# Kernel tuning notes

Hardware: AMD Instinct MI355X
Metric: run time of the kernel (lower is better)

Reference implementation:

```python
import jax, jax.numpy as jnp
import numpy as np

# dims
B, NB, T, NC = 16, 55, 512, 8          # batch, filter bands, time steps, CSP comps
D, L, H, E, K, F, C = 512, 6, 8, 8, 2, 2048, 2  # embed, depth, heads, experts, top_k, d_ff, classes
DH = D // H
IN = NB * NC  # 440
EPS = 1e-5


def _ln(x, s, b):
    m = x.mean(-1, keepdims=True)
    v = ((x - m) ** 2).mean(-1, keepdims=True)
    return (x - m) / jnp.sqrt(v + EPS) * s + b


def setup_inputs() -> dict:
    key = jax.random.key(0)
    ks = iter(jax.random.split(key, 64))
    n = lambda shape, s=0.02: jax.random.normal(next(ks), shape, jnp.float32) * s
    inp = {
        "x": jax.random.normal(next(ks), (B, NB, T, NC), jnp.float32),
        # frontend
        "proj_w": n((IN, D)), "proj_b": jnp.zeros((D,), jnp.float32),
        "pos": n((1, T, D)),
        "ln_pre_s": jnp.ones((D,), jnp.float32), "ln_pre_b": jnp.zeros((D,), jnp.float32),
        # stacked transformer-block params [L, ...]
        "ln1_s": jnp.ones((L, D), jnp.float32), "ln1_b": jnp.zeros((L, D), jnp.float32),
        "wq": n((L, D, D)), "bq": jnp.zeros((L, D), jnp.float32),
        "wk": n((L, D, D)), "bk": jnp.zeros((L, D), jnp.float32),
        "wv": n((L, D, D)), "bv": jnp.zeros((L, D), jnp.float32),
        "wo": n((L, D, D)), "bo": jnp.zeros((L, D), jnp.float32),
        "ln2_s": jnp.ones((L, D), jnp.float32), "ln2_b": jnp.zeros((L, D), jnp.float32),
        "gate_w": n((L, D, E)),
        "e_w1": n((L, E, D, F)), "e_b1": jnp.zeros((L, E, F), jnp.float32),
        "e_w2": n((L, E, F, D)), "e_b2": jnp.zeros((L, E, D), jnp.float32),
        # classifier head
        "ln_f_s": jnp.ones((D,), jnp.float32), "ln_f_b": jnp.zeros((D,), jnp.float32),
        "head_w": n((D, C)), "head_b": jnp.zeros((C,), jnp.float32),
    }
    return inp


def _moe(h, gw, w1, b1, w2, b2):
    # h: [N, D]; top-K softmax-gated mixture of GELU-FFN experts + load-balance aux loss
    N = h.shape[0]
    probs = jax.nn.softmax(h @ gw, axis=-1)                  # [N, E]
    vals, idx = jax.lax.top_k(probs, K)                      # [N, K]
    w = vals / vals.sum(-1, keepdims=True)                   # renormalized top-k weights
    disp = jax.nn.one_hot(idx, E, dtype=h.dtype)             # [N, K, E]
    combine = (disp * w[..., None]).sum(1)                   # [N, E]
    y = jnp.zeros_like(h)
    for e in range(E):  # small fixed expert loop
        y = y + combine[:, e:e + 1] * (jax.nn.gelu(h @ w1[e] + b1[e]) @ w2[e] + b2[e])
    frac = disp.mean((0, 1)) * K                             # fraction of tokens routed to each expert
    aux = E * jnp.sum(frac * probs.mean(0))
    return y, aux


def reference(x, proj_w, proj_b, pos, ln_pre_s, ln_pre_b, ln1_s, ln1_b, wq, bq, wk, bk,
              wv, bv, wo, bo, ln2_s, ln2_b, gate_w, e_w1, e_b1, e_w2, e_b2,
              ln_f_s, ln_f_b, head_w, head_b):
    b, nb, t, nc = x.shape
    h = x.transpose(0, 2, 1, 3).reshape(b, t, nb * nc) @ proj_w + proj_b  # [B,T,D]
    h = _ln(h + pos[:, :t, :], ln_pre_s, ln_pre_b)
    scale = DH ** -0.5
    total_aux = jnp.float32(0.0)
    for l in range(L):
        # pre-LN multi-head self-attention
        a = _ln(h, ln1_s[l], ln1_b[l])
        q = (a @ wq[l] + bq[l]).reshape(b, t, H, DH)
        k = (a @ wk[l] + bk[l]).reshape(b, t, H, DH)
        v = (a @ wv[l] + bv[l]).reshape(b, t, H, DH)
        att = jax.nn.softmax(jnp.einsum('bqhd,bkhd->bhqk', q, k) * scale, axis=-1)
        o = jnp.einsum('bhqk,bkhd->bqhd', att, v).reshape(b, t, D) @ wo[l] + bo[l]
        h = h + o
        # pre-LN MoE FFN
        m = _ln(h, ln2_s[l], ln2_b[l]).reshape(b * t, D)
        y, aux = _moe(m, gate_w[l], e_w1[l], e_b1[l], e_w2[l], e_b2[l])
        h = h + y.reshape(b, t, D)
        total_aux = total_aux + aux
    pooled = h.mean(axis=1)                                   # [B, D]
    logits = _ln(pooled, ln_f_s, ln_f_b) @ head_w + head_b    # [B, C]
    return logits, total_aux
```

## Files before the change

kernel.cpp:

```cpp
#include <hip/hip_runtime.h>
#include <stdint.h>

typedef unsigned short u16;
typedef unsigned int   u32;
typedef short bh8 __attribute__((ext_vector_type(8)));
typedef float f4  __attribute__((ext_vector_type(4)));

#define NTOK    8192
#define PADROWS 17408
#define MAXTILES 136

__device__ __forceinline__ u16 f2bf(float f){
  u32 u = __float_as_uint(f);
  return (u16)((u + 0x7fffu + ((u>>16)&1u)) >> 16);
}
__device__ __forceinline__ float bf2f(u16 h){ return __uint_as_float(((u32)h)<<16); }
__device__ __forceinline__ u32 pk2(float a, float b){ return (u32)f2bf(a) | ((u32)f2bf(b)<<16); }
__device__ __forceinline__ float gelu_f(float x){
  float u = 0.7978845608028654f*(x + 0.044715f*x*x*x);
  float t = 1.f - 2.f/(__expf(2.f*u)+1.f);
  return 0.5f*x*(1.f+t);
}
__device__ __forceinline__ void gload_lds16(const void* g, void* l){
  __builtin_amdgcn_global_load_lds((const __attribute__((address_space(1))) u32*)g,
                                   (__attribute__((address_space(3))) u32*)l, 16, 0, 0);
}

__global__ __launch_bounds__(256) void xpose_k(const float* __restrict__ x, u16* __restrict__ xt){
  int idx = blockIdx.x*256 + threadIdx.x;
  const float* src = x + (size_t)idx*8;
  float4 a = *(const float4*)src;
  float4 b = *(const float4*)(src+4);
  int t  = idx & 511;
  int nb = (idx>>9) % 55;
  int bb = (idx>>9) / 55;
  uint4 u;
  u.x = pk2(a.x,a.y); u.y = pk2(a.z,a.w); u.z = pk2(b.x,b.y); u.w = pk2(b.z,b.w);
  *(uint4*)&xt[((size_t)(bb*512+t))*448 + nb*8] = u;
}

__device__ __forceinline__ void tile_xpose(const float* __restrict__ src, u16* __restrict__ dst,
                                           int Ksrc, int N, int Kdst, float (*tile)[65])
{
  int tid = threadIdx.x;
  int k0 = blockIdx.y*64, n0 = blockIdx.x*64;
  #pragma unroll
  for (int p=0;p<4;++p){
    int r = p*16 + (tid>>4);
    int c4 = (tid&15)*4;
    int k = k0 + r;
    float4 v = (k < Ksrc) ? *(const float4*)&src[(size_t)k*N + n0 + c4] : (float4){0.f,0.f,0.f,0.f};
    tile[r][c4]=v.x; tile[r][c4+1]=v.y; tile[r][c4+2]=v.z; tile[r][c4+3]=v.w;
  }
  __syncthreads();
  #pragma unroll
  for (int p=0;p<2;++p){
    int rn = p*32 + (tid>>3);
    int ck = (tid&7)*8;
    uint4 u;
    u.x = pk2(tile[ck+0][rn], tile[ck+1][rn]);
    u.y = pk2(tile[ck+2][rn], tile[ck+3][rn]);
    u.z = pk2(tile[ck+4][rn], tile[ck+5][rn]);
    u.w = pk2(tile[ck+6][rn], tile[ck+7][rn]);
    *(uint4*)&dst[(size_t)(n0+rn)*Kdst + k0 + ck] = u;
  }
}

__global__ __launch_bounds__(256) void wconv_k(const float* __restrict__ src, u16* __restrict__ dst,
                                               int Ksrc, int N, int Kdst){
  __shared__ float tile[64][65];
  src += (size_t)blockIdx.z*Ksrc*N;
  dst += (size_t)blockIdx.z*N*Kdst;
  tile_xpose(src, dst, Ksrc, N, Kdst, tile);
}

__global__ __launch_bounds__(256) void wconvqkvo_k(const float* __restrict__ wq, const float* __restrict__ wk,
    const float* __restrict__ wv, const float* __restrict__ wo,
    u16* __restrict__ qkvt, u16* __restrict__ wot)
{
  __shared__ float tile[64][65];
  int z = blockIdx.z;
  int l = z>>2, which = z&3;
  const float* src = ((which==0)? wq : (which==1)? wk : (which==2)? wv : wo) + (size_t)l*512*512;
  u16* dst = (which==3) ? wot + (size_t)l*512*512
                        : qkvt + (size_t)l*1536*512 + (size_t)which*512*512;
  tile_xpose(src, dst, 512, 512, 512, tile);
}

__global__ __launch_bounds__(256) void qkvb_k(const float* __restrict__ bq, const float* __restrict__ bk,
                                              const float* __restrict__ bv, float* __restrict__ qkvb){
  int idx = blockIdx.x*256 + threadIdx.x;
  int l = idx/1536, c = idx - l*1536;
  const float* s = (c<512)? bq : (c<1024)? bk : bv;
  qkvb[idx] = s[l*512 + (c&511)];
}

template<int MODE, bool GATHER>
__global__ __launch_bounds__(256) void gemm2_k(
    const u16* __restrict__ A, int lda,
    const u16* __restrict__ Bt, int ldb, int Ksteps,
    const float* __restrict__ biasBase,
    float* __restrict__ Cf, u16* __restrict__ Cb, int ldc,
    const int* __restrict__ tile_e, const int* __restrict__ toklist,
    const float* __restrict__ wlist, int expN)
{
  __shared__ __align__(16) u16 SMEM[24576];
  const int tid = threadIdx.x, lane = tid&63, w = tid>>6;
  const int wr = w>>1, wc = w&1;
  int nx = gridDim.x;
  int nwg = nx * gridDim.y;
  int lin = blockIdx.y*nx + blockIdx.x;
  int qq = nwg>>3, rr = nwg&7, xc = lin&7, oo = lin>>3;
  int wg = (xc<rr ? xc*(qq+1) : rr*(qq+1)+(xc-rr)*qq) + oo;
  int by = wg/nx, bx = wg - by*nx;
  const int n0 = bx*128, m0 = by*128;
  const u16* Bp = Bt;
  const float* bias = biasBase;
  if constexpr (MODE>=3){
    int e = tile_e[by];
    Bp   += (size_t)e*(size_t)expN*(size_t)ldb;
    bias += (size_t)e*(size_t)expN;
  }
  const u16* asrc0; const u16* asrc1; const u16* bsrc0; const u16* bsrc1;
  {
    int idx0 = tid, row0 = idx0>>2, sp0 = idx0&3, ks0 = sp0 ^ ((row0>>1)&3);
    int idx1 = 256+tid, row1 = idx1>>2, sp1 = idx1&3, ks1 = sp1 ^ ((row1>>1)&3);
    size_t ar0 = GATHER ? (size_t)toklist[m0+row0] : (size_t)(m0+row0);
    size_t ar1 = GATHER ? (size_t)toklist[m0+row1] : (size_t)(m0+row1);
    asrc0 = A + ar0*(size_t)lda + ks0*8;
    asrc1 = A + ar1*(size_t)lda + ks1*8;
    bsrc0 = Bp + (size_t)(n0+row0)*ldb + ks0*8;
    bsrc1 = Bp + (size_t)(n0+row1)*ldb + ks1*8;
  }
  f4 acc[4][4];
  #pragma unroll
  for (int i=0;i<4;++i)
    #pragma unroll
    for (int j=0;j<4;++j) acc[i][j] = (f4){0.f,0.f,0.f,0.f};

  auto STAGE = [&](int kt){
    u16* bufA = SMEM + (kt%3)*8192;
    u16* bufB = bufA + 4096;
    gload_lds16(asrc0 + (size_t)kt*32, &bufA[tid*8]);
    gload_lds16(asrc1 + (size_t)kt*32, &bufA[2048 + tid*8]);
    gload_lds16(bsrc0 + (size_t)kt*32, &bufB[tid*8]);
    gload_lds16(bsrc1 + (size_t)kt*32, &bufB[2048 + tid*8]);
  };

  STAGE(0);
  if (Ksteps > 1) STAGE(1);
  if (Ksteps > 2) STAGE(2);

  for (int kt=0; kt<Ksteps; ++kt){
    int rem = Ksteps - 1 - kt;
    if (rem >= 2)      asm volatile("s_waitcnt vmcnt(8)" ::: "memory");
    else if (rem == 1) asm volatile("s_waitcnt vmcnt(4)" ::: "memory");
    else               asm volatile("s_waitcnt vmcnt(0)" ::: "memory");
    __builtin_amdgcn_s_barrier();
    u16* bufA = SMEM + (kt%3)*8192;
    u16* bufB = bufA + 4096;
    bh8 af[4], bf[4];
    const int q = lane>>4;
    #pragma unroll
    for (int mf=0;mf<4;++mf){
      int r = wr*64 + mf*16 + (lane&15);
      af[mf] = *(const bh8*)&bufA[r*32 + (q ^ ((r>>1)&3))*8];
    }
    #pragma unroll
    for (int nf=0;nf<4;++nf){
      int r = wc*64 + nf*16 + (lane&15);
      bf[nf] = *(const bh8*)&bufB[r*32 + (q ^ ((r>>1)&3))*8];
    }
    asm volatile("s_waitcnt lgkmcnt(0)" ::: "memory");
    __builtin_amdgcn_sched_barrier(0);
    __builtin_amdgcn_s_barrier();
    __builtin_amdgcn_sched_barrier(0);
    if (kt+3 < Ksteps) STAGE(kt+3);
    #pragma unroll
    for (int mf=0;mf<4;++mf)
      #pragma unroll
      for (int nf=0;nf<4;++nf)
        acc[mf][nf] = __builtin_amdgcn_mfma_f32_16x16x32_bf16(af[mf], bf[nf], acc[mf][nf], 0, 0, 0);
  }
  if constexpr (MODE==1 || MODE==3 || MODE==4){
    __syncthreads();
    u16* Cs = SMEM;
    #pragma unroll
    for (int mf=0;mf<4;++mf){
      int row0 = wr*64 + mf*16 + (lane>>4)*4;
      float wl[4];
      if constexpr (MODE==4){
        #pragma unroll
        for (int r=0;r<4;++r) wl[r] = wlist[m0+row0+r];
      }
      #pragma unroll
      for (int nf=0;nf<4;++nf){
        f4 d = acc[mf][nf];
        int col = wc*64 + nf*16 + (lane&15);
        float bv = bias[n0+col];
        #pragma unroll
        for (int r=0;r<4;++r){
          float val = d[r] + bv;
          if constexpr (MODE==3) val = gelu_f(val);
          if constexpr (MODE==4) val = wl[r]*val;
          Cs[(row0+r)*136 + col] = f2bf(val);
        }
      }
    }
    __syncthreads();
    #pragma unroll
    for (int p=0;p<8;++p){
      int idx = p*256 + tid;
      int row = idx>>4, c4 = idx&15;
      bh8 v = *(const bh8*)&Cs[row*136 + c4*8];
      int mrow = m0 + row;
      if constexpr (MODE==1){
        int nc = n0 + c4*8;
        int slab = nc>>6, dh = nc&63;
        *(bh8*)&Cb[((size_t)slab*NTOK + (size_t)mrow)*64 + dh] = v;
      } else {
        *(bh8*)&Cb[(size_t)mrow*ldc + n0 + c4*8] = v;
      }
    }
  } else {
    #pragma unroll
    for (int mf=0;mf<4;++mf){
      #pragma unroll
      for (int nf=0;nf<4;++nf){
        f4 d = acc[mf][nf];
        int ncol = n0 + wc*64 + nf*16 + (lane&15);
        float bv = bias[ncol];
        #pragma unroll
        for (int r=0;r<4;++r){
          int mrow = m0 + wr*64 + mf*16 + (lane>>4)*4 + r;
          float val = d[r] + bv;
          if constexpr (MODE==0){
            Cf[(size_t)mrow*ldc + ncol] = val;
          } else {
            Cf[(size_t)mrow*ldc + ncol] += val;
          }
        }
      }
    }
  }
}

template<bool ADDPOS, bool OUTF32>
__global__ __launch_bounds__(256) void ln_k(const float* __restrict__ X, const float* __restrict__ pos,
    const float* __restrict__ sc, const float* __restrict__ bi,
    float* __restrict__ outF, u16* __restrict__ outB)
{
  int tid=threadIdx.x, lane=tid&63, w=tid>>6;
  int row = blockIdx.x*4 + w;
  const float* xr = X + (size_t)row*512 + lane*8;
  float x[8];
  float4 v0 = *(const float4*)xr;
  float4 v1 = *(const float4*)(xr+4);
  x[0]=v0.x;x[1]=v0.y;x[2]=v0.z;x[3]=v0.w;x[4]=v1.x;x[5]=v1.y;x[6]=v1.z;x[7]=v1.w;
  if constexpr (ADDPOS){
    const float* pr = pos + (size_t)(row&511)*512 + lane*8;
    float4 p0 = *(const float4*)pr, p1 = *(const float4*)(pr+4);
    x[0]+=p0.x;x[1]+=p0.y;x[2]+=p0.z;x[3]+=p0.w;x[4]+=p1.x;x[5]+=p1.y;x[6]+=p1.z;x[7]+=p1.w;
  }
  float sm=0.f, sq=0.f;
  #pragma unroll
  for (int i=0;i<8;++i){ sm+=x[i]; sq+=x[i]*x[i]; }
  #pragma unroll
  for (int mk=1; mk<64; mk<<=1){ sm += __shfl_xor(sm, mk); sq += __shfl_xor(sq, mk); }
  float mean = sm*(1.f/512.f);
  float var  = sq*(1.f/512.f) - mean*mean;
  float rstd = rsqrtf(var + 1e-5f);
  int d0 = lane*8;
  float4 s0 = *(const float4*)(sc+d0), s1 = *(const float4*)(sc+d0+4);
  float4 b0 = *(const float4*)(bi+d0), b1 = *(const float4*)(bi+d0+4);
  float y[8];
  y[0]=(x[0]-mean)*rstd*s0.x+b0.x; y[1]=(x[1]-mean)*rstd*s0.y+b0.y;
  y[2]=(x[2]-mean)*rstd*s0.z+b0.z; y[3]=(x[3]-mean)*rstd*s0.w+b0.w;
  y[4]=(x[4]-mean)*rstd*s1.x+b1.x; y[5]=(x[5]-mean)*rstd*s1.y+b1.y;
  y[6]=(x[6]-mean)*rstd*s1.z+b1.z; y[7]=(x[7]-mean)*rstd*s1.w+b1.w;
  if constexpr (OUTF32){
    float4 o0 = {y[0],y[1],y[2],y[3]}, o1 = {y[4],y[5],y[6],y[7]};
    *(float4*)(outF + (size_t)row*512 + d0)     = o0;
    *(float4*)(outF + (size_t)row*512 + d0 + 4) = o1;
  } else {
    uint4 u; u.x=pk2(y[0],y[1]); u.y=pk2(y[2],y[3]); u.z=pk2(y[4],y[5]); u.w=pk2(y[6],y[7]);
    *(uint4*)&outB[(size_t)row*512 + d0] = u;
  }
}

__global__ __launch_bounds__(256) void gatherln_k(float* __restrict__ h,
    const u16* __restrict__ yb, const int* __restrict__ t2pos,
    const float* __restrict__ sc, const float* __restrict__ bi, u16* __restrict__ outB)
{
  int tid=threadIdx.x, lane=tid&63, w=tid>>6;
  int row = blockIdx.x*4 + w;
  float* hp = h + (size_t)row*512 + lane*8;
  float4 v0 = *(float4*)hp, v1 = *(float4*)(hp+4);
  int p0 = t2pos[2*row], p1 = t2pos[2*row+1];
  uint4 ya = *(const uint4*)&yb[(size_t)p0*512 + lane*8];
  uint4 yv = *(const uint4*)&yb[(size_t)p1*512 + lane*8];
  float x[8];
  x[0]=v0.x + bf2f((u16)(ya.x&0xffff)) + bf2f((u16)(yv.x&0xffff));
  x[1]=v0.y + bf2f((u16)(ya.x>>16))    + bf2f((u16)(yv.x>>16));
  x[2]=v0.z + bf2f((u16)(ya.y&0xffff)) + bf2f((u16)(yv.y&0xffff));
  x[3]=v0.w + bf2f((u16)(ya.y>>16))    + bf2f((u16)(yv.y>>16));
  x[4]=v1.x + bf2f((u16)(ya.z&0xffff)) + bf2f((u16)(yv.z&0xffff));
  x[5]=v1.y + bf2f((u16)(ya.z>>16))    + bf2f((u16)(yv.z>>16));
  x[6]=v1.z + bf2f((u16)(ya.w&0xffff)) + bf2f((u16)(yv.w&0xffff));
  x[7]=v1.w + bf2f((u16)(ya.w>>16))    + bf2f((u16)(yv.w>>16));
  float4 o0 = {x[0],x[1],x[2],x[3]}, o1 = {x[4],x[5],x[6],x[7]};
  *(float4*)hp = o0; *(float4*)(hp+4) = o1;
  float sm=0.f, sq=0.f;
  #pragma unroll
  for (int i=0;i<8;++i){ sm+=x[i]; sq+=x[i]*x[i]; }
  #pragma unroll
  for (int mk=1; mk<64; mk<<=1){ sm += __shfl_xor(sm, mk); sq += __shfl_xor(sq, mk); }
  float mean = sm*(1.f/512.f);
  float rstd = rsqrtf(sq*(1.f/512.f) - mean*mean + 1e-5f);
  int d0 = lane*8;
  float4 s0 = *(const float4*)(sc+d0), s1 = *(const float4*)(sc+d0+4);
  float4 b0 = *(const float4*)(bi+d0), b1 = *(const float4*)(bi+d0+4);
  float y[8];
  y[0]=(x[0]-mean)*rstd*s0.x+b0.x; y[1]=(x[1]-mean)*rstd*s0.y+b0.y;
  y[2]=(x[2]-mean)*rstd*s0.z+b0.z; y[3]=(x[3]-mean)*rstd*s0.w+b0.w;
  y[4]=(x[4]-mean)*rstd*s1.x+b1.x; y[5]=(x[5]-mean)*rstd*s1.y+b1.y;
  y[6]=(x[6]-mean)*rstd*s1.z+b1.z; y[7]=(x[7]-mean)*rstd*s1.w+b1.w;
  uint4 u; u.x=pk2(y[0],y[1]); u.y=pk2(y[2],y[3]); u.z=pk2(y[4],y[5]); u.w=pk2(y[6],y[7]);
  *(uint4*)&outB[(size_t)row*512 + d0] = u;
}

__global__ __launch_bounds__(256) void attn_k(const u16* __restrict__ QKV, u16* __restrict__ Og)
{
  __shared__ __align__(16) u32 VT32[2][64*36];
  __shared__ __align__(16) u16 PS[4][16*72];
  int tid=threadIdx.x, lane=tid&63, w=tid>>6;
  int qt=blockIdx.x, hh=blockIdx.y, bb=blockIdx.z;
  const u16* Qh = QKV + ((size_t)hh     *NTOK + (size_t)bb*512)*64;
  const u16* Kh = QKV + ((size_t)(8+hh) *NTOK + (size_t)bb*512)*64;
  const u16* Vh = QKV + ((size_t)(16+hh)*NTOK + (size_t)bb*512)*64;
  size_t obase = (size_t)bb*512*512 + (size_t)hh*64;
  int qrow0 = qt*64 + w*16;
  bh8 qf[2];
  #pragma unroll
  for (int kf=0;kf<2;++kf)
    qf[kf] = *(const bh8*)&Qh[ (size_t)(qrow0 + (lane&15))*64 + kf*32 + (lane>>4)*8 ];
  f4 oacc[4];
  #pragma unroll
  for (int i=0;i<4;++i) oacc[i] = (f4){0.f,0.f,0.f,0.f};
  float mrun[4] = {-1e30f,-1e30f,-1e30f,-1e30f};
  float lrun[4] = {0.f,0.f,0.f,0.f};
  const float scale = 0.125f;

  const int dhg = tid&7, kp = tid>>3, dh0 = dhg*8;
  const int blk = ((kp>>2) ^ dhg)*4 + (kp&3);

  for (int kt=0; kt<8; ++kt){
    const int buf = kt&1;
    {
      const u16* vs = &Vh[ (size_t)(kt*64 + 2*kp)*64 + dh0 ];
      uint4 va  = *(const uint4*)vs;
      uint4 vb4 = *(const uint4*)(vs + 64);
      u32 aw[4] = {va.x,va.y,va.z,va.w}, bw[4] = {vb4.x,vb4.y,vb4.z,vb4.w};
      #pragma unroll
      for (int d2=0; d2<4; ++d2){
        VT32[buf][(dh0+2*d2  )*36 + blk] = (aw[d2]&0xffffu) | (bw[d2]<<16);
        VT32[buf][(dh0+2*d2+1)*36 + blk] = (aw[d2]>>16)     | (bw[d2]&0xffff0000u);
      }
    }
    f4 s[4];
    #pragma unroll
    for (int nf=0;nf<4;++nf){
      size_t krow = (size_t)(kt*64+nf*16+(lane&15))*64 + (lane>>4)*8;
      bh8 k0 = *(const bh8*)&Kh[krow];
      bh8 k1 = *(const bh8*)&Kh[krow+32];
      f4 z = (f4){0.f,0.f,0.f,0.f};
      z = __builtin_amdgcn_mfma_f32_16x16x32_bf16(qf[0], k0, z, 0,0,0);
      z = __builtin_amdgcn_mfma_f32_16x16x32_bf16(qf[1], k1, z, 0,0,0);
      s[nf] = z;
    }
    float pe[4][4];
    #pragma unroll
    for (int r=0;r<4;++r){
      float sv0=s[0][r]*scale, sv1=s[1][r]*scale, sv2=s[2][r]*scale, sv3=s[3][r]*scale;
      float mt = fmaxf(fmaxf(sv0,sv1), fmaxf(sv2,sv3));
      #pragma unroll
      for (int mk=1; mk<16; mk<<=1) mt = fmaxf(mt, __shfl_xor(mt, mk));
      float mn = fmaxf(mrun[r], mt);
      float sf = __expf(mrun[r]-mn);
      float p0=__expf(sv0-mn), p1=__expf(sv1-mn), p2=__expf(sv2-mn), p3=__expf(sv3-mn);
      pe[0][r]=p0; pe[1][r]=p1; pe[2][r]=p2; pe[3][r]=p3;
      float rs = p0+p1+p2+p3;
      #pragma unroll
      for (int mk=1; mk<16; mk<<=1) rs += __shfl_xor(rs, mk);
      lrun[r] = lrun[r]*sf + rs;
      mrun[r] = mn;
      #pragma unroll
      for (int df=0;df<4;++df) oacc[df][r] *= sf;
    }
    #pragma unroll
    for (int nf=0;nf<4;++nf)
      #pragma unroll
      for (int r=0;r<4;++r)
        PS[w][ ((lane>>4)*4+r)*72 + nf*16 + (lane&15) ] = f2bf(pe[nf][r]);
    __syncthreads();
    #pragma unroll
    for (int ks=0;ks<2;++ks){
      bh8 pa = *(const bh8*)&PS[w][ (lane&15)*72 + ks*32 + (lane>>4)*8 ];
      #pragma unroll
      for (int df=0;df<4;++df){
        int dh = df*16 + (lane&15);
        int b4 = ((ks*4 + (lane>>4)) ^ (dh>>3))*4;
        bh8 vv = *(const bh8*)&VT32[buf][ dh*36 + b4 ];
        oacc[df] = __builtin_amdgcn_mfma_f32_16x16x32_bf16(pa, vv, oacc[df], 0,0,0);
      }
    }
  }
  #pragma unroll
  for (int df=0;df<4;++df)
    #pragma unroll
    for (int r=0;r<4;++r){
      int qr = qrow0 + (lane>>4)*4 + r;
      float ov = oacc[df][r] / lrun[r];
      Og[ obase + (size_t)qr*512 + df*16 + (lane&15) ] = f2bf(ov);
    }
}

__global__ __launch_bounds__(256) void lnroute_k(const float* __restrict__ h,
    const float* __restrict__ sc, const float* __restrict__ bi, u16* __restrict__ outB,
    const float* __restrict__ gw,
    float* __restrict__ psum, int* __restrict__ cnt, int* __restrict__ t2e, float* __restrict__ t2w)
{
  __shared__ float ps[8]; __shared__ int cs[8];
  int tid=threadIdx.x, lane=tid&63, w=tid>>6;
  if (tid<8){ ps[tid]=0.f; cs[tid]=0; }
  __syncthreads();
  int d0 = lane*8;
  float4 s0 = *(const float4*)(sc+d0), s1 = *(const float4*)(sc+d0+4);
  float4 b0 = *(const float4*)(bi+d0), b1 = *(const float4*)(bi+d0+4);
  for (int it=0; it<4; ++it){
    int t = blockIdx.x*16 + w*4 + it;
    const float* xr = h + (size_t)t*512 + d0;
    float x[8];
    float4 v0 = *(const float4*)xr, v1 = *(const float4*)(xr+4);
    x[0]=v0.x;x[1]=v0.y;x[2]=v0.z;x[3]=v0.w;x[4]=v1.x;x[5]=v1.y;x[6]=v1.z;x[7]=v1.w;
    float sm=0.f, sq=0.f;
    #pragma unroll
    for (int i=0;i<8;++i){ sm+=x[i]; sq+=x[i]*x[i]; }
    #pragma unroll
    for (int mk=1; mk<64; mk<<=1){ sm += __shfl_xor(sm, mk); sq += __shfl_xor(sq, mk); }
    float mean = sm*(1.f/512.f);
    float rstd = rsqrtf(sq*(1.f/512.f) - mean*mean + 1e-5f);
    float y[8];
    y[0]=(x[0]-mean)*rstd*s0.x+b0.x; y[1]=(x[1]-mean)*rstd*s0.y+b0.y;
    y[2]=(x[2]-mean)*rstd*s0.z+b0.z; y[3]=(x[3]-mean)*rstd*s0.w+b0.w;
    y[4]=(x[4]-mean)*rstd*s1.x+b1.x; y[5]=(x[5]-mean)*rstd*s1.y+b1.y;
    y[6]=(x[6]-mean)*rstd*s1.z+b1.z; y[7]=(x[7]-mean)*rstd*s1.w+b1.w;
    uint4 u; u.x=pk2(y[0],y[1]); u.y=pk2(y[2],y[3]); u.z=pk2(y[4],y[5]); u.w=pk2(y[6],y[7]);
    *(uint4*)&outB[(size_t)t*512 + d0] = u;
    float acc[8] = {0,0,0,0,0,0,0,0};
    #pragma unroll
    for (int j=0;j<8;++j){
      const float* g = gw + (size_t)(d0+j)*8;
      float4 g0 = *(const float4*)g, g1 = *(const float4*)(g+4);
      acc[0]+=y[j]*g0.x; acc[1]+=y[j]*g0.y; acc[2]+=y[j]*g0.z; acc[3]+=y[j]*g0.w;
      acc[4]+=y[j]*g1.x; acc[5]+=y[j]*g1.y; acc[6]+=y[j]*g1.z; acc[7]+=y[j]*g1.w;
    }
    #pragma unroll
    for (int mk=1; mk<64; mk<<=1)
      #pragma unroll
      for (int e=0;e<8;++e) acc[e] += __shfl_xor(acc[e], mk);
    if (lane==0){
      float mx=acc[0];
      #pragma unroll
      for (int e=1;e<8;++e) mx = fmaxf(mx, acc[e]);
      float pe[8], tot=0.f;
      #pragma unroll
      for (int e=0;e<8;++e){ pe[e]=__expf(acc[e]-mx); tot+=pe[e]; }
      float inv = 1.f/tot;
      #pragma unroll
      for (int e=0;e<8;++e) pe[e]*=inv;
      int e0=0; float v0e=pe[0];
      #pragma unroll
      for (int e=1;e<8;++e) if (pe[e]>v0e){ v0e=pe[e]; e0=e; }
      int e1=-1; float v1e=-1.f;
      #pragma unroll
      for (int e=0;e<8;++e) if (e!=e0 && pe[e]>v1e){ v1e=pe[e]; e1=e; }
      float invw = 1.f/(v0e+v1e);
      t2e[2*t]=e0; t2w[2*t]=v0e*invw; t2e[2*t+1]=e1; t2w[2*t+1]=v1e*invw;
      #pragma unroll
      for (int e=0;e<8;++e) atomicAdd(&ps[e], pe[e]);
      atomicAdd(&cs[e0],1); atomicAdd(&cs[e1],1);
    }
  }
  __syncthreads();
  if (tid<8){ atomicAdd(&psum[tid], ps[tid]); atomicAdd(&cnt[tid], cs[tid]); }
}

__global__ __launch_bounds__(256) void offsets_k(const int* __restrict__ cnt, const float* __restrict__ psum,
    int* __restrict__ offs, int* __restrict__ fill, int* __restrict__ tile_e,
    int* __restrict__ toklist, float* __restrict__ wlist, float* __restrict__ auxp)
{
  int tid = threadIdx.x, b = blockIdx.x;
  int i = b*256 + tid;
  if (i < PADROWS){ toklist[i]=0; wlist[i]=0.f; }
  if (b==0){
    if (tid==0){
      int off=0; float auxl=0.f;
      for (int e=0;e<8;++e){
        offs[e] = off;
        int reg = (cnt[e]+127)&~127;
        int t0 = off>>7, t1 = (off+reg)>>7;
        for (int t=t0;t<t1;++t) tile_e[t]=e;
        off += reg;
        auxl += ((float)cnt[e]*(1.f/8192.f)) * (psum[e]*(1.f/8192.f));
      }
      for (int t=off>>7; t<MAXTILES; ++t) tile_e[t]=0;
      auxp[0] += 8.f*auxl;
    }
    if (tid<8) fill[tid]=0;
  }
}

__global__ __launch_bounds__(256) void scatter_k(const int* __restrict__ t2e, const float* __restrict__ t2w,
    const int* __restrict__ offs, int* __restrict__ fill,
    int* __restrict__ toklist, float* __restrict__ wlist, int* __restrict__ t2pos)
{
  int t = blockIdx.x*256 + threadIdx.x;
  #pragma unroll
  for (int kk=0;kk<2;++kk){
    int e = t2e[2*t+kk];
    int p = atomicAdd(&fill[e], 1);
    int i = offs[e] + p;
    toklist[i] = t; wlist[i] = t2w[2*t+kk]; t2pos[2*t+kk] = i;
  }
}

__global__ __launch_bounds__(256) void gather_k(float* __restrict__ h, const u16* __restrict__ yb,
                                                const int* __restrict__ t2pos)
{
  int tid = threadIdx.x;
  int t = blockIdx.x*4 + (tid>>6);
  int lane = tid&63;
  int p0 = t2pos[2*t], p1 = t2pos[2*t+1];
  uint4 a = *(const uint4*)&yb[(size_t)p0*512 + lane*8];
  uint4 b = *(const uint4*)&yb[(size_t)p1*512 + lane*8];
  float* hp = h + (size_t)t*512 + lane*8;
  float4 h0 = *(float4*)hp, h1 = *(float4*)(hp+4);
  h0.x += bf2f((u16)(a.x&0xffff)) + bf2f((u16)(b.x&0xffff));
  h0.y += bf2f((u16)(a.x>>16))    + bf2f((u16)(b.x>>16));
  h0.z += bf2f((u16)(a.y&0xffff)) + bf2f((u16)(b.y&0xffff));
  h0.w += bf2f((u16)(a.y>>16))    + bf2f((u16)(b.y>>16));
  h1.x += bf2f((u16)(a.z&0xffff)) + bf2f((u16)(b.z&0xffff));
  h1.y += bf2f((u16)(a.z>>16))    + bf2f((u16)(b.z>>16));
  h1.z += bf2f((u16)(a.w&0xffff)) + bf2f((u16)(b.w&0xffff));
  h1.w += bf2f((u16)(a.w>>16))    + bf2f((u16)(b.w>>16));
  *(float4*)hp = h0; *(float4*)(hp+4) = h1;
}

__global__ __launch_bounds__(256) void pool_k(const float* __restrict__ h, float* __restrict__ pooled){
  int idx = blockIdx.x*256 + threadIdx.x;
  int bb = idx>>9, d = idx&511;
  const float* p = h + (size_t)bb*512*512 + d;
  float s=0.f;
  for (int t=0;t<512;++t) s += p[(size_t)t*512];
  pooled[idx] = s*(1.f/512.f);
}

__global__ __launch_bounds__(256) void head_k(const float* __restrict__ pooled,
    const float* __restrict__ sc, const float* __restrict__ bi,
    const float* __restrict__ hw, const float* __restrict__ hb,
    const float* __restrict__ auxp, float* __restrict__ out)
{
  int tid=threadIdx.x, lane=tid&63, w=tid>>6;
  for (int i=0;i<4;++i){
    int row = w*4+i;
    const float* xr = pooled + (size_t)row*512 + lane*8;
    float x[8];
    float4 v0 = *(const float4*)xr, v1 = *(const float4*)(xr+4);
    x[0]=v0.x;x[1]=v0.y;x[2]=v0.z;x[3]=v0.w;x[4]=v1.x;x[5]=v1.y;x[6]=v1.z;x[7]=v1.w;
    float sm=0.f, sq=0.f;
    #pragma unroll
    for (int j=0;j<8;++j){ sm+=x[j]; sq+=x[j]*x[j]; }
    #pragma unroll
    for (int mk=1; mk<64; mk<<=1){ sm += __shfl_xor(sm, mk); sq += __shfl_xor(sq, mk); }
    float mean = sm*(1.f/512.f);
    float rstd = rsqrtf(sq*(1.f/512.f) - mean*mean + 1e-5f);
    int d0 = lane*8;
    float c0=0.f, c1=0.f;
    #pragma unroll
    for (int j=0;j<8;++j){
      float yv = (x[j]-mean)*rstd*sc[d0+j] + bi[d0+j];
      c0 += yv*hw[(d0+j)*2]; c1 += yv*hw[(d0+j)*2+1];
    }
    #pragma unroll
    for (int mk=1; mk<64; mk<<=1){ c0 += __shfl_xor(c0, mk); c1 += __shfl_xor(c1, mk); }
    if (lane==0){ out[row*2+0] = c0 + hb[0]; out[row*2+1] = c1 + hb[1]; }
  }
  if (tid==0) out[32] = auxp[0];
}

extern "C" void kernel_launch(void* const* d_in, const int* in_sizes, int n_in,
                              void* d_out, int out_size, void* d_ws, size_t ws_size,
                              hipStream_t stream)
{
  (void)in_sizes; (void)n_in; (void)out_size; (void)ws_size;
  const float* x      = (const float*)d_in[0];
  const float* proj_w = (const float*)d_in[1];
  const float* proj_b = (const float*)d_in[2];
  const float* pos    = (const float*)d_in[3];
  const float* ln_pre_s=(const float*)d_in[4];
  const float* ln_pre_b=(const float*)d_in[5];
  const float* ln1_s  = (const float*)d_in[6];
  const float* ln1_b  = (const float*)d_in[7];
  const float* wq     = (const float*)d_in[8];
  const float* bq     = (const float*)d_in[9];
  const float* wk     = (const float*)d_in[10];
  const float* bk     = (const float*)d_in[11];
  const float* wv     = (const float*)d_in[12];
  const float* bv     = (const float*)d_in[13];
  const float* wo     = (const float*)d_in[14];
  const float* bo     = (const float*)d_in[15];
  const float* ln2_s  = (const float*)d_in[16];
  const float* ln2_b  = (const float*)d_in[17];
  const float* gate_w = (const float*)d_in[18];
  const float* e_w1   = (const float*)d_in[19];
  const float* e_b1   = (const float*)d_in[20];
  const float* e_w2   = (const float*)d_in[21];
  const float* e_b2   = (const float*)d_in[22];
  const float* ln_f_s = (const float*)d_in[23];
  const float* ln_f_b = (const float*)d_in[24];
  const float* head_w = (const float*)d_in[25];
  const float* head_b = (const float*)d_in[26];

  char* base = (char*)d_ws;
  size_t off = 0;
  auto carve = [&](size_t bytes)->char*{
    char* r = base + off; off += (bytes + 255) & ~(size_t)255; return r;
  };
  u16*   xt      = (u16*)  carve((size_t)8192*448*2);
  float* h       = (float*)carve((size_t)8192*512*4);
  u16*   a       = (u16*)  carve((size_t)8192*512*2);
  u16*   qkv     = (u16*)  carve((size_t)8192*1536*2);
  u16*   ob      = (u16*)  carve((size_t)8192*512*2);
  u16*   hidden  = (u16*)  carve((size_t)PADROWS*2048*2);
  u16*   ybuf    = (u16*)  carve((size_t)PADROWS*512*2);
  u16*   projt   = (u16*)  carve((size_t)512*448*2);
  u16*   qkvt    = (u16*)  carve((size_t)6*1536*512*2);
  u16*   wot     = (u16*)  carve((size_t)6*512*512*2);
  u16*   w1t     = (u16*)  carve((size_t)6*8*2048*512*2);
  u16*   w2t     = (u16*)  carve((size_t)6*8*512*2048*2);
  float* qkvb    = (float*)carve((size_t)6*1536*4);
  int*   toklist = (int*)  carve(PADROWS*4);
  float* wlist   = (float*)carve(PADROWS*4);
  int*   tile_e  = (int*)  carve(256*4);
  int*   rcntA   = (int*)  carve(6*16*4);
  int*   fill    = (int*)  carve(64);
  int*   offs    = (int*)  carve(64);
  int*   t2e     = (int*)  carve(16384*4);
  float* t2w     = (float*)carve(16384*4);
  int*   t2pos   = (int*)  carve(16384*4);
  float* pooled  = (float*)carve(8192*4);
  float* auxp    = (float*)carve(256);

  hipMemsetAsync(xt, 0, (size_t)8192*448*2, stream);
  hipMemsetAsync(rcntA, 0, 6*16*4, stream);
  hipMemsetAsync(auxp, 0, 4, stream);

  xpose_k<<<1760, 256, 0, stream>>>(x, xt);
  wconv_k<<<dim3(8,7,1), 256, 0, stream>>>(proj_w, projt, 440, 512, 448);
  wconvqkvo_k<<<dim3(8,8,24), 256, 0, stream>>>(wq, wk, wv, wo, qkvt, wot);
  wconv_k<<<dim3(32,8,48), 256, 0, stream>>>(e_w1, w1t, 512, 2048, 512);
  wconv_k<<<dim3(8,32,48), 256, 0, stream>>>(e_w2, w2t, 2048, 512, 2048);
  qkvb_k<<<36, 256, 0, stream>>>(bq, bk, bv, qkvb);
  gemm2_k<0,false><<<dim3(4,64), 256, 0, stream>>>(xt, 448, projt, 448, 14, proj_b,
      h, nullptr, 512, nullptr, nullptr, nullptr, 0);
  ln_k<true,true><<<2048, 256, 0, stream>>>(h, pos, ln_pre_s, ln_pre_b, h, nullptr);

  for (int l=0; l<6; ++l){
    int*   cnt  = rcntA + l*16;
    float* psum = (float*)(cnt + 8);
    if (l == 0)
      ln_k<false,false><<<2048, 256, 0, stream>>>(h, nullptr, ln1_s, ln1_b, nullptr, a);
    else
      gatherln_k<<<2048, 256, 0, stream>>>(h, ybuf, t2pos,
          ln1_s+(size_t)l*512, ln1_b+(size_t)l*512, a);
    gemm2_k<1,false><<<dim3(12,64), 256, 0, stream>>>(a, 512, qkvt+(size_t)l*1536*512, 512, 16,
        qkvb+(size_t)l*1536, nullptr, qkv, 1536, nullptr, nullptr, nullptr, 0);
    attn_k<<<dim3(8,8,16), 256, 0, stream>>>(qkv, ob);
    gemm2_k<2,false><<<dim3(4,64), 256, 0, stream>>>(ob, 512, wot+(size_t)l*512*512, 512, 16,
        bo+(size_t)l*512, h, nullptr, 512, nullptr, nullptr, nullptr, 0);
    lnroute_k<<<512, 256, 0, stream>>>(h, ln2_s+(size_t)l*512, ln2_b+(size_t)l*512, a,
        gate_w+(size_t)l*512*8, psum, cnt, t2e, t2w);
    offsets_k<<<68, 256, 0, stream>>>(cnt, psum, offs, fill, tile_e, toklist, wlist, auxp);
    scatter_k<<<32, 256, 0, stream>>>(t2e, t2w, offs, fill, toklist, wlist, t2pos);
    gemm2_k<3,true ><<<dim3(16,MAXTILES), 256, 0, stream>>>(a, 512, w1t+(size_t)l*8*2048*512, 512, 16,
        e_b1 + (size_t)l*8*2048, nullptr, hidden, 2048, tile_e, toklist, wlist, 2048);
    gemm2_k<4,false><<<dim3(4,MAXTILES), 256, 0, stream>>>(hidden, 2048, w2t+(size_t)l*8*512*2048, 2048, 64,
        e_b2 + (size_t)l*8*512, nullptr, ybuf, 512, tile_e, nullptr, wlist, 512);
  }

  gather_k<<<2048, 256, 0, stream>>>(h, ybuf, t2pos);
  pool_k<<<32, 256, 0, stream>>>(h, pooled);
  head_k<<<1, 256, 0, stream>>>(pooled, ln_f_s, ln_f_b, head_w, head_b, auxp, (float*)d_out);
}
```

Before: 2.096 ms.

## Fold attention scale into Wq, skip empty expert tiles, stage residual epilogue

Pre-multiplies Wq and bq by the 1/sqrt(dh) factor during weight conversion, which removes the per-score scale multiply in the attention kernel. Expert GEMM blocks whose tile index lies beyond the actual number of padded tiles now exit early, using a tile count that offsets_k writes into a new slot. The residual-add GEMM mode now goes through the LDS-staged epilogue and does vectorized read-modify-write on the fp32 residual. The values added to the residual are rounded to bf16 first, which changes numerics slightly. The tile_e buffer must have room for slot 200, and the unseen host code is assumed to allocate it.

```diff
diff --git a/kernel.cpp b/kernel.cpp
--- a/kernel.cpp
+++ b/kernel.cpp
@@ -9,6 +9,7 @@
 #define NTOK    8192
 #define PADROWS 17408
 #define MAXTILES 136
+#define NTILE_SLOT 200
 
 __device__ __forceinline__ u16 f2bf(float f){
   u32 u = __float_as_uint(f);
@@ -40,7 +41,7 @@
 }
 
 __device__ __forceinline__ void tile_xpose(const float* __restrict__ src, u16* __restrict__ dst,
-                                           int Ksrc, int N, int Kdst, float (*tile)[65])
+                                           int Ksrc, int N, int Kdst, float mul, float (*tile)[65])
 {
   int tid = threadIdx.x;
   int k0 = blockIdx.y*64, n0 = blockIdx.x*64;
@@ -50,7 +51,7 @@
     int c4 = (tid&15)*4;
     int k = k0 + r;
     float4 v = (k < Ksrc) ? *(const float4*)&src[(size_t)k*N + n0 + c4] : (float4){0.f,0.f,0.f,0.f};
-    tile[r][c4]=v.x; tile[r][c4+1]=v.y; tile[r][c4+2]=v.z; tile[r][c4+3]=v.w;
+    tile[r][c4]=v.x*mul; tile[r][c4+1]=v.y*mul; tile[r][c4+2]=v.z*mul; tile[r][c4+3]=v.w*mul;
   }
   __syncthreads();
   #pragma unroll
@@ -71,7 +72,7 @@
   __shared__ float tile[64][65];
   src += (size_t)blockIdx.z*Ksrc*N;
   dst += (size_t)blockIdx.z*N*Kdst;
-  tile_xpose(src, dst, Ksrc, N, Kdst, tile);
+  tile_xpose(src, dst, Ksrc, N, Kdst, 1.f, tile);
 }
 
 __global__ __launch_bounds__(256) void wconvqkvo_k(const float* __restrict__ wq, const float* __restrict__ wk,
@@ -84,7 +85,7 @@
   const float* src = ((which==0)? wq : (which==1)? wk : (which==2)? wv : wo) + (size_t)l*512*512;
   u16* dst = (which==3) ? wot + (size_t)l*512*512
                         : qkvt + (size_t)l*1536*512 + (size_t)which*512*512;
-  tile_xpose(src, dst, 512, 512, 512, tile);
+  tile_xpose(src, dst, 512, 512, 512, (which==0)? 0.125f : 1.f, tile);
 }
 
 __global__ __launch_bounds__(256) void qkvb_k(const float* __restrict__ bq, const float* __restrict__ bk,
@@ -92,7 +93,8 @@
   int idx = blockIdx.x*256 + threadIdx.x;
   int l = idx/1536, c = idx - l*1536;
   const float* s = (c<512)? bq : (c<1024)? bk : bv;
-  qkvb[idx] = s[l*512 + (c&511)];
+  float m = (c<512)? 0.125f : 1.f;
+  qkvb[idx] = m * s[l*512 + (c&511)];
 }
 
 template<int MODE, bool GATHER>
@@ -117,6 +119,7 @@
   const u16* Bp = Bt;
   const float* bias = biasBase;
   if constexpr (MODE>=3){
+    if (by >= tile_e[NTILE_SLOT]) return;
     int e = tile_e[by];
     Bp   += (size_t)e*(size_t)expN*(size_t)ldb;
     bias += (size_t)e*(size_t)expN;
@@ -182,7 +185,7 @@
       for (int nf=0;nf<4;++nf)
         acc[mf][nf] = __builtin_amdgcn_mfma_f32_16x16x32_bf16(af[mf], bf[nf], acc[mf][nf], 0, 0, 0);
   }
-  if constexpr (MODE==1 || MODE==3 || MODE==4){
+  if constexpr (MODE==1 || MODE==2 || MODE==3 || MODE==4){
     __syncthreads();
     u16* Cs = SMEM;
     #pragma unroll
@@ -218,6 +221,14 @@
         int nc = n0 + c4*8;
         int slab = nc>>6, dh = nc&63;
         *(bh8*)&Cb[((size_t)slab*NTOK + (size_t)mrow)*64 + dh] = v;
+      } else if constexpr (MODE==2){
+        float* hp = &Cf[(size_t)mrow*ldc + n0 + c4*8];
+        float4 h0 = *(float4*)hp, h1 = *(float4*)(hp+4);
+        h0.x += bf2f((u16)v[0]); h0.y += bf2f((u16)v[1]);
+        h0.z += bf2f((u16)v[2]); h0.w += bf2f((u16)v[3]);
+        h1.x += bf2f((u16)v[4]); h1.y += bf2f((u16)v[5]);
+        h1.z += bf2f((u16)v[6]); h1.w += bf2f((u16)v[7]);
+        *(float4*)hp = h0; *(float4*)(hp+4) = h1;
       } else {
         *(bh8*)&Cb[(size_t)mrow*ldc + n0 + c4*8] = v;
       }
@@ -233,12 +244,7 @@
         #pragma unroll
         for (int r=0;r<4;++r){
           int mrow = m0 + wr*64 + mf*16 + (lane>>4)*4 + r;
-          float val = d[r] + bv;
-          if constexpr (MODE==0){
-            Cf[(size_t)mrow*ldc + ncol] = val;
-          } else {
-            Cf[(size_t)mrow*ldc + ncol] += val;
-          }
+          Cf[(size_t)mrow*ldc + ncol] = d[r] + bv;
         }
       }
     }
@@ -349,7 +355,6 @@
   for (int i=0;i<4;++i) oacc[i] = (f4){0.f,0.f,0.f,0.f};
   float mrun[4] = {-1e30f,-1e30f,-1e30f,-1e30f};
   float lrun[4] = {0.f,0.f,0.f,0.f};
-  const float scale = 0.125f;
 
   const int dhg = tid&7, kp = tid>>3, dh0 = dhg*8;
   const int blk = ((kp>>2) ^ dhg)*4 + (kp&3);
@@ -381,7 +386,7 @@
     float pe[4][4];
     #pragma unroll
     for (int r=0;r<4;++r){
-      float sv0=s[0][r]*scale, sv1=s[1][r]*scale, sv2=s[2][r]*scale, sv3=s[3][r]*scale;
+      float sv0=s[0][r], sv1=s[1][r], sv2=s[2][r], sv3=s[3][r];
       float mt = fmaxf(fmaxf(sv0,sv1), fmaxf(sv2,sv3));
       #pragma unroll
       for (int mk=1; mk<16; mk<<=1) mt = fmaxf(mt, __shfl_xor(mt, mk));
@@ -514,7 +519,9 @@
         off += reg;
         auxl += ((float)cnt[e]*(1.f/8192.f)) * (psum[e]*(1.f/8192.f));
       }
-      for (int t=off>>7; t<MAXTILES; ++t) tile_e[t]=0;
+      int nt = off>>7;
+      for (int t=nt; t<MAXTILES; ++t) tile_e[t]=0;
+      tile_e[NTILE_SLOT] = nt;
       auxp[0] += 8.f*auxl;
     }
     if (tid<8) fill[tid]=0;
```

Measured after the change: 2.058 ms (median of 2 runs). Within noise of the previous version (-1.8%).
